# Performance work log

Hardware: AMD Instinct MI355X
Metric: run time of the kernel (lower is better)

Reference implementation:

```python
import jax, jax.numpy as jnp
import numpy as np

N_HEAD = 8

def setup_inputs() -> dict:
    key = jax.random.key(0)
    ks = jax.random.split(key, 5)
    N, C, T, V = 64, 128, 64, 25
    x = jax.random.normal(ks[0], (N, C, T, V), dtype=jnp.float32)
    Wa = jax.random.normal(ks[1], (C, C), dtype=jnp.float32) * (1.0 / np.sqrt(C))
    ba = jax.random.normal(ks[2], (C,), dtype=jnp.float32) * 0.01
    Wp = jax.random.normal(ks[3], (C, C), dtype=jnp.float32) * (1.0 / np.sqrt(C))
    bp = jax.random.normal(ks[4], (C,), dtype=jnp.float32) * 0.01
    temp = jnp.ones((N_HEAD, 1), dtype=jnp.float32)
    denom_bias = jnp.zeros((N_HEAD, 1, 1), dtype=jnp.float32)
    return {"x": x, "Wa": Wa, "ba": ba, "Wp": Wp, "bp": bp, "temp": temp, "denom_bias": denom_bias}

def reference(x, Wa, ba, Wp, bp, temp, denom_bias):
    # x: (N, C, T, V); eval mode (dropout = identity); residual = identity (in==out, stride==1)
    N, C, T, V = x.shape
    H = N_HEAD
    hd = C // H
    res = x
    # 1x1 conv c_attn
    w = jnp.einsum('nctv,oc->notv', x, Wa) + ba[None, :, None, None]
    # (N,H,hd,T,V) -> (N,H,T,V,hd) -> (N,H,T*V,hd)
    w = w.reshape(N, H, hd, T, V).transpose(0, 1, 3, 4, 2).reshape(N, H, T * V, hd)
    w_sq = w * w
    denom = jnp.maximum(jnp.cumsum(w_sq, axis=2), 1e-12)
    w_normed = w_sq / denom + denom_bias  # denom_bias (H,1,1) broadcasts
    tmp = jnp.sum(w_normed, axis=-1) * temp  # (N,H,L) * (H,1)
    Pi = jax.nn.softmax(tmp, axis=2)  # (N,H,L)
    dots = jnp.cumsum(w_sq * Pi[..., None], axis=2) / (jnp.cumsum(Pi, axis=2) + 1e-8)[..., None]
    attn = 1.0 / (1.0 + dots)
    y = -(w * Pi[..., None]) * attn  # (N,H,L,hd)
    y = y.reshape(N, H, T, V, hd).transpose(0, 1, 4, 2, 3).reshape(N, C, T, V)
    y = jnp.einsum('nctv,oc->notv', y, Wp) + bp[None, :, None, None]
    y = y + res
    return jax.nn.relu(y)
```

## Files before the change

kernel.cpp:

```cpp
#include <hip/hip_runtime.h>
#include <hip/hip_bf16.h>

#define N_S     64
#define C_CH    128
#define L_SEQ   1600
#define H_HEADS 8
#define HD      16
#define SEG     50
#define PADW    136
#define PADT    72

typedef __attribute__((ext_vector_type(8))) short bf16x8;
typedef __attribute__((ext_vector_type(4))) float f32x4;

__device__ inline unsigned short f2bf(float f) {
  return __builtin_bit_cast(unsigned short, __float2bfloat16(f));
}
__device__ inline float bflo(unsigned int u) { return __builtin_bit_cast(float, u << 16); }
__device__ inline float bfhi(unsigned int u) { return __builtin_bit_cast(float, u & 0xffff0000u); }

__global__ __launch_bounds__(256) void k_gemm1(const float* __restrict__ x,
                                               const float* __restrict__ Wa,
                                               const float* __restrict__ ba,
                                               unsigned short* __restrict__ w2) {
  __shared__ unsigned short was[128 * PADW];
  __shared__ unsigned short xs[128 * PADT];
  const int n = blockIdx.y;
  const int l0 = blockIdx.x * 64;
  const int t = threadIdx.x;
  const float* xn = x + (size_t)n * (C_CH * L_SEQ);

#pragma unroll
  for (int it = 0; it < 16; ++it) {
    int pos = it * 256 + t;
    int o = pos >> 5;
    int c4 = (pos & 31) << 2;
    float4 v = *reinterpret_cast<const float4*>(Wa + o * C_CH + c4);
    ushort4 u;
    u.x = f2bf(v.x); u.y = f2bf(v.y); u.z = f2bf(v.z); u.w = f2bf(v.w);
    *reinterpret_cast<ushort4*>(&was[o * PADW + c4]) = u;
  }
#pragma unroll
  for (int it = 0; it < 8; ++it) {
    int pos = it * 256 + t;
    int c = pos >> 4;
    int l4 = (pos & 15) << 2;
    float4 v = *reinterpret_cast<const float4*>(xn + (size_t)c * L_SEQ + l0 + l4);
    ushort4 u;
    u.x = f2bf(v.x); u.y = f2bf(v.y); u.z = f2bf(v.z); u.w = f2bf(v.w);
    *reinterpret_cast<ushort4*>(&xs[c * PADT + l4]) = u;
  }
  __syncthreads();

  const int wv = t >> 6;
  const int lane = t & 63;
  const int r16 = lane & 15;
  const int kg = lane >> 4;
  f32x4 acc[8];
#pragma unroll
  for (int ot = 0; ot < 8; ++ot) acc[ot] = (f32x4){0.f, 0.f, 0.f, 0.f};

#pragma unroll
  for (int ks = 0; ks < 4; ++ks) {
    bf16x8 a;
#pragma unroll
    for (int j = 0; j < 8; ++j)
      a[j] = (short)xs[(ks * 32 + kg * 8 + j) * PADT + wv * 16 + r16];
#pragma unroll
    for (int ot = 0; ot < 8; ++ot) {
      bf16x8 b = *reinterpret_cast<const bf16x8*>(&was[(ot * 16 + r16) * PADW + ks * 32 + kg * 8]);
      acc[ot] = __builtin_amdgcn_mfma_f32_16x16x32_bf16(a, b, acc[ot], 0, 0, 0);
    }
  }
#pragma unroll
  for (int ot = 0; ot < 8; ++ot) {
    float bav = ba[ot * 16 + r16];
    ushort4 u;
    u.x = f2bf(acc[ot][0] + bav);
    u.y = f2bf(acc[ot][1] + bav);
    u.z = f2bf(acc[ot][2] + bav);
    u.w = f2bf(acc[ot][3] + bav);
    size_t idx = (((size_t)n * H_HEADS + ot) * HD + r16) * L_SEQ + l0 + wv * 16 + kg * 4;
    *reinterpret_cast<ushort4*>(&w2[idx]) = u;
  }
}

__global__ __launch_bounds__(512) void k_scan(const unsigned short* __restrict__ w2,
                                              unsigned short* __restrict__ y2,
                                              const float* __restrict__ temp,
                                              const float* __restrict__ dbias) {
  __shared__ float tmp_l[L_SEQ];
  __shared__ float cbufw[8 * 680];
  __shared__ float stot[32][17];
  __shared__ float pi_seg[32];
  __shared__ float red[8];

  const int nh = blockIdx.x;
  const int h = nh & 7;
  const int t = threadIdx.x;
  const int d = t & 15;
  const int seg = t >> 4;
  const int wv = t >> 6;
  const int lane = t & 63;
  const int sl = lane >> 4;
  const int l0 = seg * SEG;
  const size_t base = ((size_t)nh * HD + d) * L_SEQ + l0;
  const float tscale = temp[h];
  const float db16 = 16.f * dbias[h];
  const float M = fmaxf((16.f + db16) * tscale, db16 * tscale);

  unsigned int vp[25];
#pragma unroll
  for (int ii = 0; ii < 25; ++ii)
    vp[ii] = *reinterpret_cast<const unsigned int*>(w2 + base + 2 * ii);

  float tot = 0.f;
#pragma unroll
  for (int ii = 0; ii < 25; ++ii) {
    float a = bflo(vp[ii]), b = bfhi(vp[ii]);
    tot += a * a + b * b;
  }
  stot[seg][d] = tot;
  __syncthreads();
  float off = 0.f;
#pragma unroll
  for (int s = 0; s < 32; ++s) { float q = stot[s][d]; if (s < seg) off += q; }

  float* cw = &cbufw[wv * 680];
  const int rsl = lane / 10;
  const int rj = lane - rsl * 10;
  float run = off;
  float sAcc = 0.f;
#pragma unroll
  for (int i0 = 0; i0 < SEG; i0 += 10) {
#pragma unroll
    for (int j = 0; j < 10; ++j) {
      int i = i0 + j;
      float v = (i & 1) ? bfhi(vp[i >> 1]) : bflo(vp[i >> 1]);
      float wsq = v * v;
      run += wsq;
      cw[(sl * 10 + j) * 17 + d] = __fdividef(wsq, fmaxf(run, 1e-12f));
    }
    __builtin_amdgcn_wave_barrier();
    if (lane < 40) {
      float a = 0.f;
#pragma unroll
      for (int dd = 0; dd < 16; ++dd) a += cw[(rsl * 10 + rj) * 17 + dd];
      float e = __expf((a + db16) * tscale - M);
      tmp_l[(4 * wv + rsl) * SEG + i0 + rj] = e;
      sAcc += e;
    }
    __builtin_amdgcn_wave_barrier();
  }
#pragma unroll
  for (int mask = 32; mask; mask >>= 1) sAcc += __shfl_xor(sAcc, mask);
  if (lane == 0) red[wv] = sAcc;
  __syncthreads();
  float S = 0.f;
#pragma unroll
  for (int i2 = 0; i2 < 8; ++i2) S += red[i2];
  const float ninvS = -1.0f / S;
  const float epsS = 1e-8f * S;

  float wp_tot = 0.f, pi_tot = 0.f;
#pragma unroll
  for (int ii = 0; ii < 25; ++ii) {
    float a = bflo(vp[ii]), b = bfhi(vp[ii]);
    float e0 = tmp_l[l0 + 2 * ii];
    float e1 = tmp_l[l0 + 2 * ii + 1];
    wp_tot += a * a * e0 + b * b * e1;
    pi_tot += e0 + e1;
  }
  stot[seg][d] = wp_tot;
  if (d == 0) pi_seg[seg] = pi_tot;
  __syncthreads();
  float wp_off = 0.f, pi_off = 0.f;
#pragma unroll
  for (int s2 = 0; s2 < 32; ++s2) {
    float vw = stot[s2][d];
    float vq = pi_seg[s2];
    if (s2 < seg) { wp_off += vw; pi_off += vq; }
  }

  {
    float run_wp = wp_off, run_pi = pi_off;
#pragma unroll
    for (int ii = 0; ii < 25; ++ii) {
      float v0 = bflo(vp[ii]), v1 = bfhi(vp[ii]);
      float e0 = tmp_l[l0 + 2 * ii];
      run_pi += e0;
      run_wp += v0 * v0 * e0;
      float dn0 = run_pi + epsS;
      float y0 = (v0 * e0) * __fdividef(dn0, dn0 + run_wp) * ninvS;
      float e1 = tmp_l[l0 + 2 * ii + 1];
      run_pi += e1;
      run_wp += v1 * v1 * e1;
      float dn1 = run_pi + epsS;
      float y1 = (v1 * e1) * __fdividef(dn1, dn1 + run_wp) * ninvS;
      vp[ii] = (unsigned int)f2bf(y0) | ((unsigned int)f2bf(y1) << 16);
    }
  }
#pragma unroll
  for (int ii = 0; ii < 25; ++ii)
    *reinterpret_cast<unsigned int*>(y2 + base + 2 * ii) = vp[ii];
}

__global__ __launch_bounds__(256) void k_gemm2(const unsigned short* __restrict__ y2,
                                               const float* __restrict__ Wp,
                                               const float* __restrict__ bp,
                                               const float* __restrict__ x,
                                               float* __restrict__ out) {
  __shared__ unsigned short wps[128 * PADW];
  __shared__ unsigned short ys[128 * PADT];
  const int n = blockIdx.y;
  const int l0 = blockIdx.x * 64;
  const int t = threadIdx.x;

#pragma unroll
  for (int it = 0; it < 16; ++it) {
    int pos = it * 256 + t;
    int o = pos >> 5;
    int c4 = (pos & 31) << 2;
    float4 v = *reinterpret_cast<const float4*>(Wp + o * C_CH + c4);
    ushort4 u;
    u.x = f2bf(v.x); u.y = f2bf(v.y); u.z = f2bf(v.z); u.w = f2bf(v.w);
    *reinterpret_cast<ushort4*>(&wps[o * PADW + c4]) = u;
  }
#pragma unroll
  for (int it = 0; it < 4; ++it) {
    int pos = it * 256 + t;
    int c = pos >> 3;
    int l8 = (pos & 7) << 3;
    uint4 v = *reinterpret_cast<const uint4*>(y2 + ((size_t)n * C_CH + c) * L_SEQ + l0 + l8);
    *reinterpret_cast<uint4*>(&ys[c * PADT + l8]) = v;
  }
  __syncthreads();

  const int wv = t >> 6;
  const int lane = t & 63;
  const int r16 = lane & 15;
  const int kg = lane >> 4;
  f32x4 acc[8];
#pragma unroll
  for (int ot = 0; ot < 8; ++ot) acc[ot] = (f32x4){0.f, 0.f, 0.f, 0.f};

#pragma unroll
  for (int ks = 0; ks < 4; ++ks) {
    bf16x8 b;
#pragma unroll
    for (int j = 0; j < 8; ++j)
      b[j] = (short)ys[(ks * 32 + kg * 8 + j) * PADT + wv * 16 + r16];
#pragma unroll
    for (int ot = 0; ot < 8; ++ot) {
      bf16x8 a = *reinterpret_cast<const bf16x8*>(&wps[(ot * 16 + r16) * PADW + ks * 32 + kg * 8]);
      acc[ot] = __builtin_amdgcn_mfma_f32_16x16x32_bf16(a, b, acc[ot], 0, 0, 0);
    }
  }
  const int gl = l0 + wv * 16 + r16;
#pragma unroll
  for (int ot = 0; ot < 8; ++ot) {
#pragma unroll
    for (int i = 0; i < 4; ++i) {
      int o = ot * 16 + kg * 4 + i;
      size_t idx = (size_t)n * (C_CH * L_SEQ) + (size_t)o * L_SEQ + gl;
      float r = acc[ot][i] + bp[o] + x[idx];
      out[idx] = fmaxf(r, 0.f);
    }
  }
}

extern "C" void kernel_launch(void* const* d_in, const int* in_sizes, int n_in,
                              void* d_out, int out_size, void* d_ws, size_t ws_size,
                              hipStream_t stream) {
  const float* x     = (const float*)d_in[0];
  const float* Wa    = (const float*)d_in[1];
  const float* ba    = (const float*)d_in[2];
  const float* Wp    = (const float*)d_in[3];
  const float* bp    = (const float*)d_in[4];
  const float* temp  = (const float*)d_in[5];
  const float* dbias = (const float*)d_in[6];
  float* out = (float*)d_out;

  unsigned short* w2 = (unsigned short*)d_ws;
  unsigned short* y2 = w2 + (size_t)N_S * H_HEADS * L_SEQ * HD;

  k_gemm1<<<dim3(L_SEQ / 64, N_S), 256, 0, stream>>>(x, Wa, ba, w2);
  k_scan<<<N_S * H_HEADS, 512, 0, stream>>>(w2, y2, temp, dbias);
  k_gemm2<<<dim3(L_SEQ / 64, N_S), 256, 0, stream>>>(y2, Wp, bp, x, out);
}
```

Measured before the change: 77.05 us.

## Split scan into 64 segments per head with 1024-thread blocks

The scan kernel now uses 64 segments of 25 elements per (sample, head) instead of 32 segments of 50, doubling threads per block to 1024. Segment indices are interleaved across waves, and odd-offset segments handle the unaligned bf16 pair with a shifted load and a split store. The aim is to shorten each thread's serial scan and raise parallelism, since the grid has only 512 blocks. In exchange it adds prefix loops over 64 segments, 16-bit scalar edge stores and odd-aligned memory accesses.

```diff
diff --git a/kernel.cpp b/kernel.cpp
--- a/kernel.cpp
+++ b/kernel.cpp
@@ -6,7 +6,8 @@
 #define L_SEQ   1600
 #define H_HEADS 8
 #define HD      16
-#define SEG     50
+#define SEGN    64
+#define SEGL    25
 #define PADW    136
 #define PADT    72
 
@@ -18,6 +19,9 @@
 }
 __device__ inline float bflo(unsigned int u) { return __builtin_bit_cast(float, u << 16); }
 __device__ inline float bfhi(unsigned int u) { return __builtin_bit_cast(float, u & 0xffff0000u); }
+__device__ inline unsigned int pk(float a, float b) {
+  return (unsigned int)f2bf(a) | ((unsigned int)f2bf(b) << 16);
+}
 
 __global__ __launch_bounds__(256) void k_gemm1(const float* __restrict__ x,
                                                const float* __restrict__ Wa,
@@ -85,69 +89,80 @@
   }
 }
 
-__global__ __launch_bounds__(512) void k_scan(const unsigned short* __restrict__ w2,
-                                              unsigned short* __restrict__ y2,
-                                              const float* __restrict__ temp,
-                                              const float* __restrict__ dbias) {
+__global__ __launch_bounds__(1024, 4) void k_scan(const unsigned short* __restrict__ w2,
+                                                  unsigned short* __restrict__ y2,
+                                                  const float* __restrict__ temp,
+                                                  const float* __restrict__ dbias) {
   __shared__ float tmp_l[L_SEQ];
-  __shared__ float cbufw[8 * 680];
-  __shared__ float stot[32][17];
-  __shared__ float pi_seg[32];
-  __shared__ float red[8];
+  __shared__ float cbufw[16 * 340];
+  __shared__ float stot[SEGN][17];
+  __shared__ float pi_seg[SEGN];
+  __shared__ float red[16];
 
   const int nh = blockIdx.x;
   const int h = nh & 7;
   const int t = threadIdx.x;
   const int d = t & 15;
-  const int seg = t >> 4;
+  const int lane = t & 63;
   const int wv = t >> 6;
-  const int lane = t & 63;
+  const int OFF = wv >> 3;
+  const int wl = wv & 7;
   const int sl = lane >> 4;
-  const int l0 = seg * SEG;
-  const size_t base = ((size_t)nh * HD + d) * L_SEQ + l0;
+  const int seg = 8 * wl + 2 * sl + OFF;
+  const int l0 = seg * SEGL;
+  const int g0 = (nh * HD + d) * L_SEQ + l0;
   const float tscale = temp[h];
   const float db16 = 16.f * dbias[h];
   const float M = fmaxf((16.f + db16) * tscale, db16 * tscale);
 
-  unsigned int vp[25];
-#pragma unroll
-  for (int ii = 0; ii < 25; ++ii)
-    vp[ii] = *reinterpret_cast<const unsigned int*>(w2 + base + 2 * ii);
+  unsigned int dw[13];
+  {
+    const unsigned int* src = reinterpret_cast<const unsigned int*>(w2 + (g0 - OFF));
+#pragma unroll
+    for (int ii = 0; ii < 13; ++ii) dw[ii] = src[ii];
+  }
+  float v[SEGL];
+  if (OFF == 0) {
+#pragma unroll
+    for (int i = 0; i < SEGL; ++i)
+      v[i] = (i & 1) ? bfhi(dw[i >> 1]) : bflo(dw[i >> 1]);
+  } else {
+#pragma unroll
+    for (int i = 0; i < SEGL; ++i)
+      v[i] = ((i + 1) & 1) ? bfhi(dw[(i + 1) >> 1]) : bflo(dw[(i + 1) >> 1]);
+  }
 
   float tot = 0.f;
 #pragma unroll
-  for (int ii = 0; ii < 25; ++ii) {
-    float a = bflo(vp[ii]), b = bfhi(vp[ii]);
-    tot += a * a + b * b;
-  }
+  for (int i = 0; i < SEGL; ++i) tot += v[i] * v[i];
   stot[seg][d] = tot;
   __syncthreads();
   float off = 0.f;
 #pragma unroll
-  for (int s = 0; s < 32; ++s) { float q = stot[s][d]; if (s < seg) off += q; }
-
-  float* cw = &cbufw[wv * 680];
-  const int rsl = lane / 10;
-  const int rj = lane - rsl * 10;
+  for (int s = 0; s < SEGN; ++s) { float q = stot[s][d]; if (s < seg) off += q; }
+
+  float* cw = &cbufw[wv * 340];
+  const int rsl = lane / 5;
+  const int rj = lane - rsl * 5;
+  const int rseg = 8 * wl + 2 * rsl + OFF;
   float run = off;
   float sAcc = 0.f;
 #pragma unroll
-  for (int i0 = 0; i0 < SEG; i0 += 10) {
-#pragma unroll
-    for (int j = 0; j < 10; ++j) {
-      int i = i0 + j;
-      float v = (i & 1) ? bfhi(vp[i >> 1]) : bflo(vp[i >> 1]);
-      float wsq = v * v;
+  for (int i0 = 0; i0 < SEGL; i0 += 5) {
+#pragma unroll
+    for (int j = 0; j < 5; ++j) {
+      float vv = v[i0 + j];
+      float wsq = vv * vv;
       run += wsq;
-      cw[(sl * 10 + j) * 17 + d] = __fdividef(wsq, fmaxf(run, 1e-12f));
+      cw[(sl * 5 + j) * 17 + d] = __fdividef(wsq, fmaxf(run, 1e-12f));
     }
     __builtin_amdgcn_wave_barrier();
-    if (lane < 40) {
+    if (lane < 20) {
       float a = 0.f;
 #pragma unroll
-      for (int dd = 0; dd < 16; ++dd) a += cw[(rsl * 10 + rj) * 17 + dd];
+      for (int dd = 0; dd < 16; ++dd) a += cw[(rsl * 5 + rj) * 17 + dd];
       float e = __expf((a + db16) * tscale - M);
-      tmp_l[(4 * wv + rsl) * SEG + i0 + rj] = e;
+      tmp_l[rseg * SEGL + i0 + rj] = e;
       sAcc += e;
     }
     __builtin_amdgcn_wave_barrier();
@@ -158,25 +173,23 @@
   __syncthreads();
   float S = 0.f;
 #pragma unroll
-  for (int i2 = 0; i2 < 8; ++i2) S += red[i2];
+  for (int i2 = 0; i2 < 16; ++i2) S += red[i2];
   const float ninvS = -1.0f / S;
   const float epsS = 1e-8f * S;
 
   float wp_tot = 0.f, pi_tot = 0.f;
 #pragma unroll
-  for (int ii = 0; ii < 25; ++ii) {
-    float a = bflo(vp[ii]), b = bfhi(vp[ii]);
-    float e0 = tmp_l[l0 + 2 * ii];
-    float e1 = tmp_l[l0 + 2 * ii + 1];
-    wp_tot += a * a * e0 + b * b * e1;
-    pi_tot += e0 + e1;
+  for (int i = 0; i < SEGL; ++i) {
+    float e = tmp_l[l0 + i];
+    wp_tot += v[i] * v[i] * e;
+    pi_tot += e;
   }
   stot[seg][d] = wp_tot;
   if (d == 0) pi_seg[seg] = pi_tot;
   __syncthreads();
   float wp_off = 0.f, pi_off = 0.f;
 #pragma unroll
-  for (int s2 = 0; s2 < 32; ++s2) {
+  for (int s2 = 0; s2 < SEGN; ++s2) {
     float vw = stot[s2][d];
     float vq = pi_seg[s2];
     if (s2 < seg) { wp_off += vw; pi_off += vq; }
@@ -185,24 +198,27 @@
   {
     float run_wp = wp_off, run_pi = pi_off;
 #pragma unroll
-    for (int ii = 0; ii < 25; ++ii) {
-      float v0 = bflo(vp[ii]), v1 = bfhi(vp[ii]);
-      float e0 = tmp_l[l0 + 2 * ii];
-      run_pi += e0;
-      run_wp += v0 * v0 * e0;
-      float dn0 = run_pi + epsS;
-      float y0 = (v0 * e0) * __fdividef(dn0, dn0 + run_wp) * ninvS;
-      float e1 = tmp_l[l0 + 2 * ii + 1];
-      run_pi += e1;
-      run_wp += v1 * v1 * e1;
-      float dn1 = run_pi + epsS;
-      float y1 = (v1 * e1) * __fdividef(dn1, dn1 + run_wp) * ninvS;
-      vp[ii] = (unsigned int)f2bf(y0) | ((unsigned int)f2bf(y1) << 16);
-    }
-  }
-#pragma unroll
-  for (int ii = 0; ii < 25; ++ii)
-    *reinterpret_cast<unsigned int*>(y2 + base + 2 * ii) = vp[ii];
+    for (int i = 0; i < SEGL; ++i) {
+      float e = tmp_l[l0 + i];
+      run_pi += e;
+      float wsq = v[i] * v[i];
+      run_wp += wsq * e;
+      float dn = run_pi + epsS;
+      v[i] = (v[i] * e) * __fdividef(dn, dn + run_wp) * ninvS;
+    }
+  }
+
+  if (OFF == 0) {
+    unsigned int* dst = reinterpret_cast<unsigned int*>(y2 + g0);
+#pragma unroll
+    for (int ii = 0; ii < 12; ++ii) dst[ii] = pk(v[2 * ii], v[2 * ii + 1]);
+    y2[g0 + 24] = f2bf(v[24]);
+  } else {
+    y2[g0] = f2bf(v[0]);
+    unsigned int* dst = reinterpret_cast<unsigned int*>(y2 + g0 + 1);
+#pragma unroll
+    for (int ii = 0; ii < 12; ++ii) dst[ii] = pk(v[1 + 2 * ii], v[2 + 2 * ii]);
+  }
 }
 
 __global__ __launch_bounds__(256) void k_gemm2(const unsigned short* __restrict__ y2,
@@ -285,6 +301,6 @@
   unsigned short* y2 = w2 + (size_t)N_S * H_HEADS * L_SEQ * HD;
 
   k_gemm1<<<dim3(L_SEQ / 64, N_S), 256, 0, stream>>>(x, Wa, ba, w2);
-  k_scan<<<N_S * H_HEADS, 512, 0, stream>>>(w2, y2, temp, dbias);
+  k_scan<<<N_S * H_HEADS, 1024, 0, stream>>>(w2, y2, temp, dbias);
   k_gemm2<<<dim3(L_SEQ / 64, N_S), 256, 0, stream>>>(y2, Wp, bp, x, out);
 }
```

Result: slower. 85.37 us (+10.8%).

## Replace LDS head-dim reduction with DPP adds and parallel segment prefix scans

Applied to the files above, without the earlier changes.

The scan kernel now reduces the per-position sum across the 16 head-dim lanes with DPP row-shift adds instead of staging values through shared memory under wave barriers. The exp values are kept in registers as packed bf16 rather than in a shared tmp buffer. The serial 32-segment offset loops are replaced by shuffle-based prefix scans. The aim is less LDS traffic and synchronisation and lower shared-memory use, allowing higher occupancy. In exchange it adds DPP reduction across 16 lanes, bf16 rounding of the softmax weights, and a 1/16 rescale of the sum.

```diff
diff --git a/kernel.cpp b/kernel.cpp
--- a/kernel.cpp
+++ b/kernel.cpp
@@ -6,7 +6,8 @@
 #define L_SEQ   1600
 #define H_HEADS 8
 #define HD      16
-#define SEG     50
+#define SEGN    32
+#define SEGL    50
 #define PADW    136
 #define PADT    72
 
@@ -18,6 +19,15 @@
 }
 __device__ inline float bflo(unsigned int u) { return __builtin_bit_cast(float, u << 16); }
 __device__ inline float bfhi(unsigned int u) { return __builtin_bit_cast(float, u & 0xffff0000u); }
+__device__ inline unsigned int pk(float a, float b) {
+  return (unsigned int)f2bf(a) | ((unsigned int)f2bf(b) << 16);
+}
+
+template <int CTRL>
+__device__ inline float dppadd(float x) {
+  int r = __builtin_amdgcn_update_dpp(0, __builtin_bit_cast(int, x), CTRL, 0xF, 0xF, true);
+  return x + __builtin_bit_cast(float, r);
+}
 
 __global__ __launch_bounds__(256) void k_gemm1(const float* __restrict__ x,
                                                const float* __restrict__ Wa,
@@ -85,34 +95,31 @@
   }
 }
 
-__global__ __launch_bounds__(512) void k_scan(const unsigned short* __restrict__ w2,
-                                              unsigned short* __restrict__ y2,
-                                              const float* __restrict__ temp,
-                                              const float* __restrict__ dbias) {
-  __shared__ float tmp_l[L_SEQ];
-  __shared__ float cbufw[8 * 680];
-  __shared__ float stot[32][17];
-  __shared__ float pi_seg[32];
+__global__ __launch_bounds__(512, 4) void k_scan(const unsigned short* __restrict__ w2,
+                                                 unsigned short* __restrict__ y2,
+                                                 const float* __restrict__ temp,
+                                                 const float* __restrict__ dbias) {
+  __shared__ float stot[SEGN][17];
   __shared__ float red[8];
 
   const int nh = blockIdx.x;
   const int h = nh & 7;
   const int t = threadIdx.x;
   const int d = t & 15;
+  const int lane = t & 63;
+  const int wv = t >> 6;
   const int seg = t >> 4;
-  const int wv = t >> 6;
-  const int lane = t & 63;
-  const int sl = lane >> 4;
-  const int l0 = seg * SEG;
-  const size_t base = ((size_t)nh * HD + d) * L_SEQ + l0;
+  const size_t base = ((size_t)nh * HD + d) * L_SEQ + seg * SEGL;
   const float tscale = temp[h];
   const float db16 = 16.f * dbias[h];
   const float M = fmaxf((16.f + db16) * tscale, db16 * tscale);
 
   unsigned int vp[25];
-#pragma unroll
-  for (int ii = 0; ii < 25; ++ii)
-    vp[ii] = *reinterpret_cast<const unsigned int*>(w2 + base + 2 * ii);
+  {
+    const unsigned int* src = reinterpret_cast<const unsigned int*>(w2 + base);
+#pragma unroll
+    for (int ii = 0; ii < 25; ++ii) vp[ii] = src[ii];
+  }
 
   float tot = 0.f;
 #pragma unroll
@@ -122,87 +129,99 @@
   }
   stot[seg][d] = tot;
   __syncthreads();
-  float off = 0.f;
-#pragma unroll
-  for (int s = 0; s < 32; ++s) { float q = stot[s][d]; if (s < seg) off += q; }
-
-  float* cw = &cbufw[wv * 680];
-  const int rsl = lane / 10;
-  const int rj = lane - rsl * 10;
+#pragma unroll
+  for (int it = 0; it < 2; ++it) {
+    int col = wv + it * 8;
+    float val = (lane < 32) ? stot[lane][col] : 0.f;
+#pragma unroll
+    for (int sh = 1; sh < 32; sh <<= 1) {
+      float nv = __shfl_up(val, sh);
+      if (lane >= sh) val += nv;
+    }
+    if (lane < 32) stot[lane][col] = val;
+  }
+  __syncthreads();
+  const float off = stot[seg][d] - tot;
+
+  unsigned int ep[25];
   float run = off;
-  float sAcc = 0.f;
-#pragma unroll
-  for (int i0 = 0; i0 < SEG; i0 += 10) {
-#pragma unroll
-    for (int j = 0; j < 10; ++j) {
-      int i = i0 + j;
-      float v = (i & 1) ? bfhi(vp[i >> 1]) : bflo(vp[i >> 1]);
-      float wsq = v * v;
-      run += wsq;
-      cw[(sl * 10 + j) * 17 + d] = __fdividef(wsq, fmaxf(run, 1e-12f));
-    }
-    __builtin_amdgcn_wave_barrier();
-    if (lane < 40) {
-      float a = 0.f;
-#pragma unroll
-      for (int dd = 0; dd < 16; ++dd) a += cw[(rsl * 10 + rj) * 17 + dd];
-      float e = __expf((a + db16) * tscale - M);
-      tmp_l[(4 * wv + rsl) * SEG + i0 + rj] = e;
-      sAcc += e;
-    }
-    __builtin_amdgcn_wave_barrier();
-  }
-#pragma unroll
-  for (int mask = 32; mask; mask >>= 1) sAcc += __shfl_xor(sAcc, mask);
-  if (lane == 0) red[wv] = sAcc;
-  __syncthreads();
-  float S = 0.f;
-#pragma unroll
-  for (int i2 = 0; i2 < 8; ++i2) S += red[i2];
+  float sAcc = 0.f, wpAcc = 0.f;
+  float eprev = 0.f;
+#pragma unroll
+  for (int i = 0; i < SEGL; ++i) {
+    float v = (i & 1) ? bfhi(vp[i >> 1]) : bflo(vp[i >> 1]);
+    float wsq = v * v;
+    run += wsq;
+    float c = __fdividef(wsq, fmaxf(run, 1e-12f));
+    c = dppadd<0x128>(c);
+    c = dppadd<0x124>(c);
+    c = dppadd<0x122>(c);
+    c = dppadd<0x121>(c);
+    float e = __expf((c + db16) * tscale - M);
+    sAcc += e;
+    wpAcc = fmaf(wsq, e, wpAcc);
+    if (i & 1) ep[i >> 1] = pk(eprev, e); else eprev = e;
+  }
+  {
+    float s = sAcc;
+#pragma unroll
+    for (int mask = 32; mask; mask >>= 1) s += __shfl_xor(s, mask);
+    if (lane == 0) red[wv] = s;
+  }
+  __syncthreads();
+  float S16 = 0.f;
+#pragma unroll
+  for (int i2 = 0; i2 < 8; ++i2) S16 += red[i2];
+  const float S = S16 * 0.0625f;
   const float ninvS = -1.0f / S;
   const float epsS = 1e-8f * S;
 
-  float wp_tot = 0.f, pi_tot = 0.f;
-#pragma unroll
-  for (int ii = 0; ii < 25; ++ii) {
-    float a = bflo(vp[ii]), b = bfhi(vp[ii]);
-    float e0 = tmp_l[l0 + 2 * ii];
-    float e1 = tmp_l[l0 + 2 * ii + 1];
-    wp_tot += a * a * e0 + b * b * e1;
-    pi_tot += e0 + e1;
-  }
-  stot[seg][d] = wp_tot;
-  if (d == 0) pi_seg[seg] = pi_tot;
-  __syncthreads();
-  float wp_off = 0.f, pi_off = 0.f;
-#pragma unroll
-  for (int s2 = 0; s2 < 32; ++s2) {
-    float vw = stot[s2][d];
-    float vq = pi_seg[s2];
-    if (s2 < seg) { wp_off += vw; pi_off += vq; }
-  }
+  stot[seg][d] = wpAcc;
+  if (d == 0) stot[seg][16] = sAcc;
+  __syncthreads();
+#pragma unroll
+  for (int it = 0; it < 2; ++it) {
+    int col = wv + it * 8;
+    float val = (lane < 32) ? stot[lane][col] : 0.f;
+#pragma unroll
+    for (int sh = 1; sh < 32; sh <<= 1) {
+      float nv = __shfl_up(val, sh);
+      if (lane >= sh) val += nv;
+    }
+    if (lane < 32) stot[lane][col] = val;
+  }
+  if (wv == 0) {
+    float val = (lane < 32) ? stot[lane][16] : 0.f;
+#pragma unroll
+    for (int sh = 1; sh < 32; sh <<= 1) {
+      float nv = __shfl_up(val, sh);
+      if (lane >= sh) val += nv;
+    }
+    if (lane < 32) stot[lane][16] = val;
+  }
+  __syncthreads();
+  const float wp_off = stot[seg][d] - wpAcc;
+  const float pi_off = stot[seg][16] - sAcc;
 
   {
     float run_wp = wp_off, run_pi = pi_off;
-#pragma unroll
-    for (int ii = 0; ii < 25; ++ii) {
-      float v0 = bflo(vp[ii]), v1 = bfhi(vp[ii]);
-      float e0 = tmp_l[l0 + 2 * ii];
-      run_pi += e0;
-      run_wp += v0 * v0 * e0;
-      float dn0 = run_pi + epsS;
-      float y0 = (v0 * e0) * __fdividef(dn0, dn0 + run_wp) * ninvS;
-      float e1 = tmp_l[l0 + 2 * ii + 1];
-      run_pi += e1;
-      run_wp += v1 * v1 * e1;
-      float dn1 = run_pi + epsS;
-      float y1 = (v1 * e1) * __fdividef(dn1, dn1 + run_wp) * ninvS;
-      vp[ii] = (unsigned int)f2bf(y0) | ((unsigned int)f2bf(y1) << 16);
-    }
-  }
-#pragma unroll
-  for (int ii = 0; ii < 25; ++ii)
-    *reinterpret_cast<unsigned int*>(y2 + base + 2 * ii) = vp[ii];
+    float ylo = 0.f;
+#pragma unroll
+    for (int i = 0; i < SEGL; ++i) {
+      float v = (i & 1) ? bfhi(vp[i >> 1]) : bflo(vp[i >> 1]);
+      float e = (i & 1) ? bfhi(ep[i >> 1]) : bflo(ep[i >> 1]);
+      run_pi += e;
+      run_wp = fmaf(v * v, e, run_wp);
+      float dn = run_pi + epsS;
+      float y = (v * e) * __fdividef(dn, dn + run_wp) * ninvS;
+      if (i & 1) vp[i >> 1] = pk(ylo, y); else ylo = y;
+    }
+  }
+  {
+    unsigned int* dst = reinterpret_cast<unsigned int*>(y2 + base);
+#pragma unroll
+    for (int ii = 0; ii < 25; ++ii) dst[ii] = vp[ii];
+  }
 }
 
 __global__ __launch_bounds__(256) void k_gemm2(const unsigned short* __restrict__ y2,
```

After: 76.85 us. About the same (-0.3%).
